# Kernel optimization log

Hardware: AMD Instinct MI355X
Metric: run time of the kernel (lower is better)

The kernel has to match this reference:

```python
import jax, jax.numpy as jnp
import numpy as np

B, N, D, OUT = 8192, 256, 128, 10  # batch, input_dim (sites), bond_dim, output_dim
LOCAL = 2  # local physical dimension (hardcoded in source)


def setup_inputs() -> dict:
    key = jax.random.key(0)
    ks = jax.random.split(key, 6)
    scale = 1.0 / np.sqrt(D)  # stable variant of source's 0.1 init (keeps 256-site product O(1))
    x = jax.random.normal(ks[0], (B, N), dtype=jnp.float32)
    first = jax.random.normal(ks[1], (1, LOCAL, D), dtype=jnp.float32) * scale   # site 0: (1,2,D)
    mid = jax.random.normal(ks[2], (N - 2, D, LOCAL, D), dtype=jnp.float32) * scale  # sites 1..N-2
    last = jax.random.normal(ks[3], (D, LOCAL, 1), dtype=jnp.float32) * scale    # site N-1: (D,2,1)
    w = jax.random.normal(ks[4], (OUT, 1), dtype=jnp.float32) * 0.1  # nn.Linear(1, OUT) weight
    b = jnp.zeros((OUT,), dtype=jnp.float32)                          # nn.Linear(1, OUT) bias
    return {"x": x, "first": first, "mid": mid, "last": last, "w": w, "b": b}


def _feature_map(x):
    # per-sample min/max normalization over the feature axis, then (cos, sin) embedding
    x_min = jnp.min(x, axis=1, keepdims=True)
    x_max = jnp.max(x, axis=1, keepdims=True)
    x_norm = (x - x_min) / (x_max - x_min + 1e-6)
    ang = (np.pi / 2) * x_norm
    return jnp.stack([jnp.cos(ang), jnp.sin(ang)], axis=2)  # [B, N, 2]


def reference(x, first, mid, last, w, b):
    phi = _feature_map(x)  # [B, N, 2]
    # site 0: left[b, r] = sum_d first[0, d, r] * phi[b, 0, d]
    left = jnp.einsum('dr,bd->br', first[0], phi[:, 0])  # [B, D]
    # sites 1..N-2 via scan: left <- sum_{l,d} left[b,l] * M[l,d,r] * phi[b,i,d]
    phi_mid = jnp.swapaxes(phi[:, 1:-1], 0, 1)  # [N-2, B, 2]

    def step(left, inputs):
        M, p = inputs  # M: [D, 2, D], p: [B, 2]
        left = jnp.einsum('bl,ldr,bd->br', left, M, p)
        return left, None

    left, _ = jax.lax.scan(step, left, (mid, phi_mid))  # [B, D]
    # last site: scalar[b] = sum_{l,d} left[b,l] * last[l,d,0] * phi[b,N-1,d]
    scalar = jnp.einsum('bl,ld,bd->b', left, last[:, :, 0], phi[:, -1])  # [B]
    # nn.Linear(1, OUT): logits = scalar * w^T + b
    logits = scalar[:, None] * w[:, 0][None, :] + b  # [B, OUT]
    return logits
```

## Files before the change

### kernel.cpp

```cpp
#include <hip/hip_runtime.h>


typedef _Float16 v8h __attribute__((ext_vector_type(8)));
typedef _Float16 h2  __attribute__((ext_vector_type(2)));
typedef float    v4f __attribute__((ext_vector_type(4)));

#define PI_HALF 1.5707963267948966f
#define SITE_U4 4096
#define TOFF_U4 (127*4096)

union U4H8 { uint4 u; v8h h; };

__device__ __forceinline__ v4f mfma16h(uint4 a, uint4 b, v4f c){
  U4H8 ua, ub; ua.u = a; ub.u = b;
  return __builtin_amdgcn_mfma_f32_16x16x32_f16(ua.h, ub.h, c, 0, 0, 0);
}
__device__ __forceinline__ unsigned pack2h(float lo, float hi){
  h2 p; p[0] = (_Float16)lo; p[1] = (_Float16)hi;
  return __builtin_bit_cast(unsigned, p);
}
__device__ __forceinline__ unsigned short f16b(float v){
  return __builtin_bit_cast(unsigned short, (_Float16)v);
}

__global__ __launch_bounds__(256) void repack_mid(const float* __restrict__ mid,
                                                  unsigned short* __restrict__ wsB){
  const int bid = blockIdx.x;
  if (bid < 508){
    int idx  = bid * 256 + threadIdx.x;
    int lg   = idx & 15;
    int nt   = (idx >> 4) & 7;
    int kt   = (idx >> 7) & 3;
    int d    = (idx >> 9) & 1;
    int site = idx >> 10;
    int q    = lg >> 2;
    int n0   = 16*nt + 4*(lg & 3);
    const float* src = mid + ((size_t)(site*128 + 32*kt + 8*q)*2 + d)*128 + n0;
    float V[8][4];
    #pragma unroll
    for (int j = 0; j < 8; ++j){
      float4 a = *(const float4*)(src + (size_t)j*256);
      V[j][0]=a.x; V[j][1]=a.y; V[j][2]=a.z; V[j][3]=a.w;
    }
    uint4* dst = (uint4*)wsB + ((((size_t)site*2 + d)*4 + kt)*8 + nt)*64
               + 16*q + 4*(lg & 3);
    #pragma unroll
    for (int t = 0; t < 4; ++t){
      uint4 o;
      o.x = pack2h(V[0][t], V[1][t]);
      o.y = pack2h(V[2][t], V[3][t]);
      o.z = pack2h(V[4][t], V[5][t]);
      o.w = pack2h(V[6][t], V[7][t]);
      dst[t] = o;
    }
  } else {
    int idx  = (bid - 508) * 256 + threadIdx.x;
    int lg   = idx & 15;
    int kt   = (idx >> 4) & 3;
    int am   = (idx >> 6) & 7;
    int d    = (idx >> 9) & 1;
    int srel = idx >> 10;
    int site = 127 + srel;
    int q    = lg >> 2;
    int m0   = 16*am + 4*(lg & 3);
    int k0   = 32*kt + 8*q;
    uint4* dst = (uint4*)wsB + TOFF_U4
               + ((((size_t)srel*2 + d)*8 + am)*4 + kt)*64 + 16*q + 4*(lg & 3);
    #pragma unroll
    for (int mp = 0; mp < 4; ++mp){
      const float* src = mid + ((size_t)((site*128 + m0 + mp)*2) + d)*128 + k0;
      float4 a = *(const float4*)(src);
      float4 b = *(const float4*)(src + 4);
      uint4 o;
      o.x = pack2h(a.x, a.y);
      o.y = pack2h(a.z, a.w);
      o.z = pack2h(b.x, b.y);
      o.w = pack2h(b.z, b.w);
      dst[mp] = o;
    }
  }
}

__global__ __launch_bounds__(512, 2) void mps_main(
    const float* __restrict__ x,
    const float* __restrict__ first,
    const unsigned short* __restrict__ wsBv,
    const float* __restrict__ lastw,
    const float* __restrict__ wlin,
    const float* __restrict__ blin,
    float* __restrict__ out)
{
  __shared__ unsigned phiT[256*36];
  __shared__ unsigned Af[2*2*4*64*4];
  __shared__ unsigned Rf[2*4*2*64*4];
  __shared__ float Rcomb[128*33];
  __shared__ float scal[32];

  const int tid  = threadIdx.x;
  const int gblk = blockIdx.x;
  const int w    = tid >> 6;
  const int lane = tid & 63;
  const int r    = lane & 15;
  const int q    = lane >> 4;
  const int rh   = r >> 3;
  const int rowbase = gblk * 32;
  const int physL = lane ^ ((lane >> 3) & 7);

  {
    const int row = tid >> 4;
    const int c0  = (tid & 15) * 16;
    const float4* xp = (const float4*)(x + (size_t)(rowbase + row) * 256 + c0);
    float xv[16];
    float vmin = 3.0e38f, vmax = -3.0e38f;
    #pragma unroll
    for (int c = 0; c < 4; ++c){
      float4 u = xp[c];
      xv[c*4+0] = u.x; xv[c*4+1] = u.y; xv[c*4+2] = u.z; xv[c*4+3] = u.w;
      vmin = fminf(vmin, fminf(fminf(u.x,u.y), fminf(u.z,u.w)));
      vmax = fmaxf(vmax, fmaxf(fmaxf(u.x,u.y), fmaxf(u.z,u.w)));
    }
    #pragma unroll
    for (int m = 1; m < 16; m <<= 1){
      vmin = fminf(vmin, __shfl_xor(vmin, m));
      vmax = fmaxf(vmax, __shfl_xor(vmax, m));
    }
    const float sc = PI_HALF / (vmax - vmin + 1e-6f);
    #pragma unroll
    for (int j = 0; j < 16; ++j){
      float a = (xv[j] - vmin) * sc;
      phiT[(c0 + j)*36 + row] = pack2h(__cosf(a), __sinf(a));
    }
  }
  __syncthreads();

  uint4 B0[16], B1[16];
  if (w < 4){
    const uint4* bp = (const uint4*)wsBv;
    #pragma unroll
    for (int d = 0; d < 2; ++d)
      #pragma unroll
      for (int kt = 0; kt < 4; ++kt)
        #pragma unroll
        for (int nb = 0; nb < 2; ++nb)
          B0[(d*4+kt)*2+nb] = bp[(size_t)((d*4 + kt)*8 + 2*w + nb)*64 + lane];
  } else {
    const int ww = w - 4;
    const uint4* bp = (const uint4*)wsBv + TOFF_U4 + (size_t)126 * SITE_U4;
    #pragma unroll
    for (int d = 0; d < 2; ++d)
      #pragma unroll
      for (int mtl = 0; mtl < 2; ++mtl)
        #pragma unroll
        for (int kt = 0; kt < 4; ++kt)
          B0[(d*2+mtl)*4+kt] = bp[(size_t)((d*8 + 2*ww + mtl)*4 + kt)*64 + lane];
  }

  if (w < 4){
    float f0[8], f1[8];
    #pragma unroll
    for (int j = 0; j < 8; ++j){
      int l = 32*w + 8*q + j;
      f0[j] = first[l]; f1[j] = first[128 + l];
    }
    #pragma unroll
    for (int mt = 0; mt < 2; ++mt){
      h2 ph0 = __builtin_bit_cast(h2, phiT[0*36 + 16*mt + r]);
      const float c0 = (float)ph0[0], s0 = (float)ph0[1];
      uint4 o;
      o.x = pack2h(f0[0]*c0 + f1[0]*s0, f0[1]*c0 + f1[1]*s0);
      o.y = pack2h(f0[2]*c0 + f1[2]*s0, f0[3]*c0 + f1[3]*s0);
      o.z = pack2h(f0[4]*c0 + f1[4]*s0, f0[5]*c0 + f1[5]*s0);
      o.w = pack2h(f0[6]*c0 + f1[6]*s0, f0[7]*c0 + f1[7]*s0);
      *(uint4*)&Af[((mt*4 + w)*64 + physL)*4] = o;
    }
  } else {
    const int ww = w - 4;
    float g0[8], g1[8];
    #pragma unroll
    for (int j = 0; j < 8; ++j){
      int rr = 32*ww + 8*q + j;
      float2 gg = *(const float2*)(lastw + 2*rr);
      g0[j] = gg.x; g1[j] = gg.y;
    }
    #pragma unroll
    for (int nt = 0; nt < 2; ++nt){
      h2 p5 = __builtin_bit_cast(h2, phiT[255*36 + 16*nt + r]);
      const float cb = (float)p5[0], sb = (float)p5[1];
      uint4 o;
      o.x = pack2h(g0[0]*cb + g1[0]*sb, g0[1]*cb + g1[1]*sb);
      o.y = pack2h(g0[2]*cb + g1[2]*sb, g0[3]*cb + g1[3]*sb);
      o.z = pack2h(g0[4]*cb + g1[4]*sb, g0[5]*cb + g1[5]*sb);
      o.w = pack2h(g0[6]*cb + g1[6]*sb, g0[7]*cb + g1[7]*sb);
      *(uint4*)&Rf[((ww*2 + nt)*64 + physL)*4] = o;
    }
  }

  auto body = [&](int t, uint4 (&Fc)[16], uint4 (&Fn)[16]){
    __syncthreads();
    float vf[2][2][4];

    if (w < 4){
      {
        const int soff = (t < 126) ? (t + 1) : 0;
        const uint4* bp = (const uint4*)wsBv + (size_t)soff * SITE_U4;
        #pragma unroll
        for (int d = 0; d < 2; ++d)
          #pragma unroll
          for (int kt = 0; kt < 4; ++kt)
            #pragma unroll
            for (int nb = 0; nb < 2; ++nb)
              Fn[(d*4+kt)*2+nb] = bp[(size_t)((d*4 + kt)*8 + 2*w + nb)*64 + lane];
      }
      v4f ac0[2][2] = {};
      v4f ac1[2][2] = {};
      const unsigned* Ab = &Af[(t & 1) * 2048];
      #pragma unroll
      for (int kt = 0; kt < 4; ++kt){
        uint4 a0 = *(const uint4*)&Ab[((0*4 + kt)*64 + physL)*4];
        uint4 a1 = *(const uint4*)&Ab[((1*4 + kt)*64 + physL)*4];
        #pragma unroll
        for (int nb = 0; nb < 2; ++nb){
          ac0[0][nb] = mfma16h(a0, Fc[(0*4+kt)*2+nb], ac0[0][nb]);
          ac0[1][nb] = mfma16h(a1, Fc[(0*4+kt)*2+nb], ac0[1][nb]);
          ac1[0][nb] = mfma16h(a0, Fc[(1*4+kt)*2+nb], ac1[0][nb]);
          ac1[1][nb] = mfma16h(a1, Fc[(1*4+kt)*2+nb], ac1[1][nb]);
        }
      }
      if (t < 126){
        unsigned short* Wb = (unsigned short*)&Af[((t+1) & 1) * 2048];
        #pragma unroll
        for (int mt = 0; mt < 2; ++mt){
          uint4 phiu = *(const uint4*)&phiT[(t+1)*36 + 16*mt + 4*q];
          const unsigned pr[4] = {phiu.x, phiu.y, phiu.z, phiu.w};
          #pragma unroll
          for (int nb = 0; nb < 2; ++nb){
            const int S0 = 32*nb + 16*rh + 4*q;
            const int X  = 4*nb + 2*rh + (q >> 1);
            #pragma unroll
            for (int reg = 0; reg < 4; ++reg){
              h2 ph = __builtin_bit_cast(h2, pr[reg]);
              float v = (float)ph[0]*ac0[mt][nb][reg]
                      + (float)ph[1]*ac1[mt][nb][reg];
              Wb[((mt*4 + w)*64 + ((S0 + reg) ^ X))*8 + (r & 7)] = f16b(v);
            }
          }
        }
      } else {
        #pragma unroll
        for (int mt = 0; mt < 2; ++mt){
          uint4 phiu = *(const uint4*)&phiT[127*36 + 16*mt + 4*q];
          const unsigned pr[4] = {phiu.x, phiu.y, phiu.z, phiu.w};
          #pragma unroll
          for (int nb = 0; nb < 2; ++nb)
            #pragma unroll
            for (int reg = 0; reg < 4; ++reg){
              h2 ph = __builtin_bit_cast(h2, pr[reg]);
              vf[mt][nb][reg] = (float)ph[0]*ac0[mt][nb][reg]
                              + (float)ph[1]*ac1[mt][nb][reg];
            }
        }
      }
    } else {
      const int ww = w - 4;
      {
        const int srel = (t < 126) ? (125 - t) : 0;
        const uint4* bp = (const uint4*)wsBv + TOFF_U4 + (size_t)srel * SITE_U4;
        #pragma unroll
        for (int d = 0; d < 2; ++d)
          #pragma unroll
          for (int mtl = 0; mtl < 2; ++mtl)
            #pragma unroll
            for (int kt = 0; kt < 4; ++kt)
              Fn[(d*2+mtl)*4+kt] = bp[(size_t)((d*8 + 2*ww + mtl)*4 + kt)*64 + lane];
      }
      v4f ac0[2][2] = {};
      v4f ac1[2][2] = {};
      const unsigned* Rb = &Rf[(t & 1) * 2048];
      #pragma unroll
      for (int kt = 0; kt < 4; ++kt){
        uint4 b0 = *(const uint4*)&Rb[((kt*2 + 0)*64 + physL)*4];
        uint4 b1 = *(const uint4*)&Rb[((kt*2 + 1)*64 + physL)*4];
        #pragma unroll
        for (int mtl = 0; mtl < 2; ++mtl){
          ac0[mtl][0] = mfma16h(Fc[(0*2+mtl)*4+kt], b0, ac0[mtl][0]);
          ac0[mtl][1] = mfma16h(Fc[(0*2+mtl)*4+kt], b1, ac0[mtl][1]);
          ac1[mtl][0] = mfma16h(Fc[(1*2+mtl)*4+kt], b0, ac1[mtl][0]);
          ac1[mtl][1] = mfma16h(Fc[(1*2+mtl)*4+kt], b1, ac1[mtl][1]);
        }
      }
      const int ps = 254 - t;
      if (t < 126){
        unsigned short* Wr = (unsigned short*)&Rf[((t+1) & 1) * 2048];
        #pragma unroll
        for (int nb = 0; nb < 2; ++nb){
          h2 ph = __builtin_bit_cast(h2, phiT[ps*36 + 16*nb + r]);
          const float cb = (float)ph[0], sb = (float)ph[1];
          #pragma unroll
          for (int mtl = 0; mtl < 2; ++mtl){
            const int S0 = 32*mtl + 16*(q >> 1) + r;
            const int phys = S0 ^ ((S0 >> 3) & 7);
            #pragma unroll
            for (int reg = 0; reg < 4; ++reg){
              float v = cb*ac0[mtl][nb][reg] + sb*ac1[mtl][nb][reg];
              Wr[((ww*2 + nb)*64 + phys)*8 + ((4*q + reg) & 7)] = f16b(v);
            }
          }
        }
      } else {
        #pragma unroll
        for (int nb = 0; nb < 2; ++nb){
          h2 ph = __builtin_bit_cast(h2, phiT[ps*36 + 16*nb + r]);
          const float cb = (float)ph[0], sb = (float)ph[1];
          #pragma unroll
          for (int mtl = 0; mtl < 2; ++mtl)
            #pragma unroll
            for (int reg = 0; reg < 4; ++reg){
              float v = cb*ac0[mtl][nb][reg] + sb*ac1[mtl][nb][reg];
              int l = 32*ww + 16*mtl + 4*q + reg;
              Rcomb[l*33 + 16*nb + r] = v;
            }
        }
      }
    }

    if (t == 126){
      if (tid < 32) scal[tid] = 0.0f;
      __syncthreads();
      if (w < 4){
        float p[2][4] = {};
        #pragma unroll
        for (int mt = 0; mt < 2; ++mt)
          #pragma unroll
          for (int nb = 0; nb < 2; ++nb){
            const int l = 32*w + 16*nb + r;
            #pragma unroll
            for (int reg = 0; reg < 4; ++reg)
              p[mt][reg] += vf[mt][nb][reg] * Rcomb[l*33 + 16*mt + 4*q + reg];
          }
        #pragma unroll
        for (int m = 1; m < 16; m <<= 1)
          #pragma unroll
          for (int mt = 0; mt < 2; ++mt)
            #pragma unroll
            for (int reg = 0; reg < 4; ++reg)
              p[mt][reg] += __shfl_xor(p[mt][reg], m);
        if (r == 0){
          #pragma unroll
          for (int mt = 0; mt < 2; ++mt)
            #pragma unroll
            for (int reg = 0; reg < 4; ++reg)
              atomicAdd(&scal[16*mt + 4*q + reg], p[mt][reg]);
        }
      }
      __syncthreads();
      for (int t2 = tid; t2 < 320; t2 += 512){
        int bb = t2 / 10, o = t2 - bb*10;
        out[(size_t)(rowbase + bb)*10 + o] = scal[bb]*wlin[o] + blin[o];
      }
    }
  };

  #pragma unroll 1
  for (int t = 0; t < 126; t += 2){
    body(t,     B0, B1);
    body(t + 1, B1, B0);
  }
  body(126, B0, B1);
}

extern "C" void kernel_launch(void* const* d_in, const int* in_sizes, int n_in,
                              void* d_out, int out_size, void* d_ws, size_t ws_size,
                              hipStream_t stream){
  (void)in_sizes; (void)n_in; (void)out_size; (void)ws_size;
  const float* x     = (const float*)d_in[0];
  const float* first = (const float*)d_in[1];
  const float* mid   = (const float*)d_in[2];
  const float* lastw = (const float*)d_in[3];
  const float* wlin  = (const float*)d_in[4];
  const float* blin  = (const float*)d_in[5];
  float* o            = (float*)d_out;
  unsigned short* wsB = (unsigned short*)d_ws;

  hipLaunchKernelGGL(repack_mid, dim3(1016), dim3(256), 0, stream, mid, wsB);
  hipLaunchKernelGGL(mps_main,   dim3(256),  dim3(512), 0, stream,
                     x, first, wsB, lastw, wlin, blin, o);
}
```

Baseline: 262.1 us.

## Fuse weight repack into main kernel via cooperative launch and grid sync

Merges the separate repack kernel into the main MPS kernel. Each block first repacks its share of the mid-site tensors and computes phi, then all blocks meet at a grid-wide cooperative sync before the chain contraction. This removes one kernel launch and the gap between the two kernels. In exchange it needs a cooperative launch, with 256 blocks of 512 threads co-resident, and adds grid-barrier overhead.

```diff
diff --git a/kernel.cpp b/kernel.cpp
--- a/kernel.cpp
+++ b/kernel.cpp
@@ -1,4 +1,7 @@
 #include <hip/hip_runtime.h>
+#include <hip/hip_cooperative_groups.h>
+
+namespace cg = cooperative_groups;
 
 
 typedef _Float16 v8h __attribute__((ext_vector_type(8)));
@@ -23,72 +26,70 @@
   return __builtin_bit_cast(unsigned short, (_Float16)v);
 }
 
-__global__ __launch_bounds__(256) void repack_mid(const float* __restrict__ mid,
-                                                  unsigned short* __restrict__ wsB){
-  const int bid = blockIdx.x;
-  if (bid < 508){
-    int idx  = bid * 256 + threadIdx.x;
-    int lg   = idx & 15;
-    int nt   = (idx >> 4) & 7;
-    int kt   = (idx >> 7) & 3;
-    int d    = (idx >> 9) & 1;
-    int site = idx >> 10;
-    int q    = lg >> 2;
-    int n0   = 16*nt + 4*(lg & 3);
-    const float* src = mid + ((size_t)(site*128 + 32*kt + 8*q)*2 + d)*128 + n0;
-    float V[8][4];
-    #pragma unroll
-    for (int j = 0; j < 8; ++j){
-      float4 a = *(const float4*)(src + (size_t)j*256);
-      V[j][0]=a.x; V[j][1]=a.y; V[j][2]=a.z; V[j][3]=a.w;
-    }
-    uint4* dst = (uint4*)wsB + ((((size_t)site*2 + d)*4 + kt)*8 + nt)*64
-               + 16*q + 4*(lg & 3);
-    #pragma unroll
-    for (int t = 0; t < 4; ++t){
-      uint4 o;
-      o.x = pack2h(V[0][t], V[1][t]);
-      o.y = pack2h(V[2][t], V[3][t]);
-      o.z = pack2h(V[4][t], V[5][t]);
-      o.w = pack2h(V[6][t], V[7][t]);
-      dst[t] = o;
-    }
-  } else {
-    int idx  = (bid - 508) * 256 + threadIdx.x;
-    int lg   = idx & 15;
-    int kt   = (idx >> 4) & 3;
-    int am   = (idx >> 6) & 7;
-    int d    = (idx >> 9) & 1;
-    int srel = idx >> 10;
-    int site = 127 + srel;
-    int q    = lg >> 2;
-    int m0   = 16*am + 4*(lg & 3);
-    int k0   = 32*kt + 8*q;
-    uint4* dst = (uint4*)wsB + TOFF_U4
-               + ((((size_t)srel*2 + d)*8 + am)*4 + kt)*64 + 16*q + 4*(lg & 3);
-    #pragma unroll
-    for (int mp = 0; mp < 4; ++mp){
-      const float* src = mid + ((size_t)((site*128 + m0 + mp)*2) + d)*128 + k0;
-      float4 a = *(const float4*)(src);
-      float4 b = *(const float4*)(src + 4);
-      uint4 o;
-      o.x = pack2h(a.x, a.y);
-      o.y = pack2h(a.z, a.w);
-      o.z = pack2h(b.x, b.y);
-      o.w = pack2h(b.z, b.w);
-      dst[mp] = o;
-    }
-  }
-}
-
-__global__ __launch_bounds__(512, 2) void mps_main(
+__device__ __forceinline__ void repack_fwd_unit(int idx, const float* __restrict__ mid,
+                                                unsigned short* __restrict__ wsB){
+  int lg   = idx & 15;
+  int nt   = (idx >> 4) & 7;
+  int kt   = (idx >> 7) & 3;
+  int d    = (idx >> 9) & 1;
+  int site = idx >> 10;
+  int q    = lg >> 2;
+  int n0   = 16*nt + 4*(lg & 3);
+  const float* src = mid + ((size_t)(site*128 + 32*kt + 8*q)*2 + d)*128 + n0;
+  float V[8][4];
+  #pragma unroll
+  for (int j = 0; j < 8; ++j){
+    float4 a = *(const float4*)(src + (size_t)j*256);
+    V[j][0]=a.x; V[j][1]=a.y; V[j][2]=a.z; V[j][3]=a.w;
+  }
+  uint4* dst = (uint4*)wsB + ((((size_t)site*2 + d)*4 + kt)*8 + nt)*64
+             + 16*q + 4*(lg & 3);
+  #pragma unroll
+  for (int t = 0; t < 4; ++t){
+    uint4 o;
+    o.x = pack2h(V[0][t], V[1][t]);
+    o.y = pack2h(V[2][t], V[3][t]);
+    o.z = pack2h(V[4][t], V[5][t]);
+    o.w = pack2h(V[6][t], V[7][t]);
+    dst[t] = o;
+  }
+}
+__device__ __forceinline__ void repack_bwd_unit(int idx, const float* __restrict__ mid,
+                                                unsigned short* __restrict__ wsB){
+  int lg   = idx & 15;
+  int kt   = (idx >> 4) & 3;
+  int am   = (idx >> 6) & 7;
+  int d    = (idx >> 9) & 1;
+  int srel = idx >> 10;
+  int site = 127 + srel;
+  int q    = lg >> 2;
+  int m0   = 16*am + 4*(lg & 3);
+  int k0   = 32*kt + 8*q;
+  uint4* dst = (uint4*)wsB + TOFF_U4
+             + ((((size_t)srel*2 + d)*8 + am)*4 + kt)*64 + 16*q + 4*(lg & 3);
+  #pragma unroll
+  for (int mp = 0; mp < 4; ++mp){
+    const float* src = mid + ((size_t)((site*128 + m0 + mp)*2) + d)*128 + k0;
+    float4 a = *(const float4*)(src);
+    float4 b = *(const float4*)(src + 4);
+    uint4 o;
+    o.x = pack2h(a.x, a.y);
+    o.y = pack2h(a.z, a.w);
+    o.z = pack2h(b.x, b.y);
+    o.w = pack2h(b.z, b.w);
+    dst[mp] = o;
+  }
+}
+
+__global__ __launch_bounds__(512, 2) void mps_fused(
     const float* __restrict__ x,
     const float* __restrict__ first,
-    const unsigned short* __restrict__ wsBv,
+    unsigned short* __restrict__ wsBv,
     const float* __restrict__ lastw,
     const float* __restrict__ wlin,
     const float* __restrict__ blin,
-    float* __restrict__ out)
+    float* __restrict__ out,
+    const float* __restrict__ mid)
 {
   __shared__ unsigned phiT[256*36];
   __shared__ unsigned Af[2*2*4*64*4];
@@ -107,6 +108,14 @@
   const int physL = lane ^ ((lane >> 3) & 7);
 
   {
+    const int u = gblk * 512 + tid;
+    if (u < 130048){
+      repack_fwd_unit(u, mid, wsBv);
+      repack_bwd_unit(u, mid, wsBv);
+    }
+  }
+
+  {
     const int row = tid >> 4;
     const int c0  = (tid & 15) * 16;
     const float4* xp = (const float4*)(x + (size_t)(rowbase + row) * 256 + c0);
@@ -131,7 +140,9 @@
       phiT[(c0 + j)*36 + row] = pack2h(__cosf(a), __sinf(a));
     }
   }
-  __syncthreads();
+
+  __threadfence();
+  cg::this_grid().sync();
 
   uint4 B0[16], B1[16];
   if (w < 4){
@@ -381,7 +392,8 @@
   float* o            = (float*)d_out;
   unsigned short* wsB = (unsigned short*)d_ws;
 
-  hipLaunchKernelGGL(repack_mid, dim3(1016), dim3(256), 0, stream, mid, wsB);
-  hipLaunchKernelGGL(mps_main,   dim3(256),  dim3(512), 0, stream,
-                     x, first, wsB, lastw, wlin, blin, o);
-}
+  void* args[] = { (void*)&x, (void*)&first, (void*)&wsB, (void*)&lastw,
+                   (void*)&wlin, (void*)&blin, (void*)&o, (void*)&mid };
+  hipLaunchCooperativeKernel(reinterpret_cast<void*>(mps_fused),
+                             dim3(256), dim3(512), args, 0, stream);
+}
```

After: 388.3 us. 48.1% more time.
